# Kernel tuning notes

Measured on AMD Instinct MI355X. Metric: run time of the kernel, lower is better.

## Reference

```python
import jax, jax.numpy as jnp
import numpy as np
import math

B, T, D, H = 4, 1024, 1024, 16
DK = D // H
TAU_THRESH = 0.3


def setup_inputs() -> dict:
    key = jax.random.key(0)
    ks = jax.random.split(key, 13)
    s = 1.0 / math.sqrt(D)
    return {
        "x": jax.random.normal(ks[0], (B, T, D), dtype=jnp.float32),
        "Wq": jax.random.normal(ks[1], (D, D), dtype=jnp.float32) * s,
        "bq": jax.random.normal(ks[2], (D,), dtype=jnp.float32) * s,
        "Wk": jax.random.normal(ks[3], (D, D), dtype=jnp.float32) * s,
        "bk": jax.random.normal(ks[4], (D,), dtype=jnp.float32) * s,
        "Wv": jax.random.normal(ks[5], (D, D), dtype=jnp.float32) * s,
        "bv": jax.random.normal(ks[6], (D,), dtype=jnp.float32) * s,
        "Wo": jax.random.normal(ks[7], (D, D), dtype=jnp.float32) * s,
        "bo": jax.random.normal(ks[8], (D,), dtype=jnp.float32) * s,
        "Wg1": jax.random.normal(ks[9], (1, D), dtype=jnp.float32) * s,
        "bg1": jax.random.normal(ks[10], (1,), dtype=jnp.float32) * s,
        "Wg2": jax.random.normal(ks[11], (1, D), dtype=jnp.float32) * s,
        "bg2": jax.random.normal(ks[12], (1,), dtype=jnp.float32) * s,
    }


def reference(x, Wq, bq, Wk, bk, Wv, bv, Wo, bo, Wg1, bg1, Wg2, bg2):
    b, t, d = x.shape
    # projections (torch Linear: y = x @ W.T + b)
    Q = (x @ Wq.T + bq).reshape(b, t, H, DK).transpose(0, 2, 1, 3)  # [B,H,T,dk]
    K = (x @ Wk.T + bk).reshape(b, t, H, DK).transpose(0, 2, 1, 3)
    V = (x @ Wv.T + bv).reshape(b, t, H, DK).transpose(0, 2, 1, 3)
    scores = jnp.einsum("bhqd,bhkd->bhqk", Q, K) / math.sqrt(DK)  # [B,H,T,T]
    # confidence gates from first-token query context [B, H*dk] = [B, D]
    context = Q[:, :, 0, :].reshape(b, d)
    q1 = jax.nn.sigmoid(context @ Wg1.T + bg1)  # [B,1]
    q2 = jax.nn.sigmoid(context @ Wg2.T + bg2)  # [B,1]
    c = jnp.clip(q1 * q2, 1e-8, 1.0)            # [B,1]
    tau = jnp.where(c < TAU_THRESH, 1.0 / c, jnp.ones_like(c)).reshape(b, 1, 1, 1)
    p = jax.nn.softmax(scores / tau, axis=-1)
    cb = c.reshape(b, 1, 1, 1)
    p_gated = cb * p + (1.0 - cb) * (1.0 / t)
    u = jnp.mean(1.0 - c, axis=-1, keepdims=True)  # [B,1]
    attn_out = jnp.einsum("bhqk,bhkd->bhqd", p_gated, V)
    attn_out = attn_out.transpose(0, 2, 1, 3).reshape(b, t, d)
    output = attn_out @ Wo.T + bo
    return output, u
```

## Files before the change

### kernel.cpp

```cpp
#include <hip/hip_runtime.h>
#include <stdint.h>

typedef short bf16x8 __attribute__((ext_vector_type(8)));
typedef float f32x4 __attribute__((ext_vector_type(4)));

#define MFMA_BF16(a, b, c) __builtin_amdgcn_mfma_f32_16x16x32_bf16((a), (b), (c), 0, 0, 0)

__device__ __forceinline__ short f2bf(float x) {
  union { float f; uint32_t u; } v; v.f = x;
  uint32_t r = (v.u + 0x7FFFu + ((v.u >> 16) & 1u)) >> 16;
  return (short)r;
}
__device__ __forceinline__ uint32_t rnd_bf_hi(float x) {
  union { float f; uint32_t u; } v; v.f = x;
  return v.u + 0x7FFFu + ((v.u >> 16) & 1u);
}
__device__ __forceinline__ uint32_t pack2bf(float a, float b) {
  return __builtin_amdgcn_perm(rnd_bf_hi(b), rnd_bf_hi(a), 0x07060302);
}
__device__ __forceinline__ float bfbits2f(uint32_t b16) {
  union { uint32_t u; float f; } v; v.u = b16 << 16; return v.f;
}
__device__ __forceinline__ float fexp2(float x) {
#if __has_builtin(__builtin_amdgcn_exp2f)
  return __builtin_amdgcn_exp2f(x);
#else
  return __expf(x * 0.6931471805599453f);
#endif
}
__device__ __forceinline__ void async16(const void* g, void* l) {
  __builtin_amdgcn_global_load_lds(
      (const __attribute__((address_space(1))) uint32_t*)g,
      (__attribute__((address_space(3))) uint32_t*)l, 16, 0, 0);
}

__global__ __launch_bounds__(256) void prep_k(
    const float* __restrict__ x, const float* __restrict__ Wq,
    const float* __restrict__ Wk, const float* __restrict__ Wv,
    const float* __restrict__ Wo, const float* __restrict__ bq,
    short* __restrict__ xb, short* __restrict__ Wqb, short* __restrict__ Wkb,
    short* __restrict__ Wvb, short* __restrict__ Wob, float* __restrict__ ctx) {
  __shared__ float xs[1024];
  const int bid = blockIdx.x;
  const int tid = threadIdx.x;
  if (bid < 8192) {
    const float* src; short* dst; int idx;
    if (bid < 4096) {
      src = x; dst = xb; idx = (bid << 8) + tid;
    } else {
      const int r = bid - 4096;
      const int z = r >> 10;
      src = (z == 0) ? Wq : (z == 1) ? Wk : (z == 2) ? Wv : Wo;
      dst = (z == 0) ? Wqb : (z == 1) ? Wkb : (z == 2) ? Wvb : Wob;
      idx = ((r & 1023) << 8) + tid;
    }
    float4 v = ((const float4*)src)[idx];
    short4 o;
    o.x = f2bf(v.x); o.y = f2bf(v.y); o.z = f2bf(v.z); o.w = f2bf(v.w);
    ((short4*)dst)[idx] = o;
  } else {
    const int r = bid - 8192;
    const int b = r >> 4;
    const int n0 = (r & 15) << 6;
    for (int i = tid; i < 1024; i += 256) xs[i] = x[b * 1048576 + i];
    __syncthreads();
    const int w = tid >> 6, lane = tid & 63;
    const float4* xv4 = (const float4*)xs;
    for (int rr = 0; rr < 16; ++rr) {
      const int n = n0 + (w << 4) + rr;
      const float4* wrow = (const float4*)(Wq + n * 1024);
      float p = 0.f;
#pragma unroll
      for (int c2 = 0; c2 < 4; ++c2) {
        float4 wv = wrow[lane + (c2 << 6)];
        float4 xv = xv4[lane + (c2 << 6)];
        p += xv.x * wv.x + xv.y * wv.y + xv.z * wv.z + xv.w * wv.w;
      }
#pragma unroll
      for (int off = 32; off; off >>= 1) p += __shfl_xor(p, off);
      if (lane == 0) ctx[b * 1024 + n] = p + bq[n];
    }
  }
}

__global__ __launch_bounds__(256) void gates_fin(const float* __restrict__ ctx,
                                                 const float* __restrict__ Wg1,
                                                 const float* __restrict__ bg1,
                                                 const float* __restrict__ Wg2,
                                                 const float* __restrict__ bg2,
                                                 float* __restrict__ gates,
                                                 float* __restrict__ u_out) {
  __shared__ float red[16];
  const int tid = threadIdx.x, w = tid >> 6, lane = tid & 63;
  for (int b = 0; b < 4; ++b) {
    float4 cv = ((const float4*)(ctx + b * 1024))[tid];
    float4 w1 = ((const float4*)Wg1)[tid];
    float4 w2 = ((const float4*)Wg2)[tid];
    float p1 = cv.x * w1.x + cv.y * w1.y + cv.z * w1.z + cv.w * w1.w;
    float p2 = cv.x * w2.x + cv.y * w2.y + cv.z * w2.z + cv.w * w2.w;
#pragma unroll
    for (int off = 32; off; off >>= 1) { p1 += __shfl_xor(p1, off); p2 += __shfl_xor(p2, off); }
    if (lane == 0) { red[w] = p1; red[8 + w] = p2; }
    __syncthreads();
    if (tid == 0) {
      float g1 = red[0] + red[1] + red[2] + red[3] + bg1[0];
      float g2 = red[8] + red[9] + red[10] + red[11] + bg2[0];
      float q1 = 1.f / (1.f + expf(-g1));
      float q2 = 1.f / (1.f + expf(-g2));
      float c = fminf(fmaxf(q1 * q2, 1e-8f), 1.0f);
      gates[b * 2 + 0] = c;
      gates[b * 2 + 1] = (c < 0.3f ? c : 1.0f) * 0.125f * 1.4426950408889634f;
      u_out[b] = 1.0f - c;
    }
    __syncthreads();
  }
}

__global__ __launch_bounds__(256) void gemm_qkv(
    const short* __restrict__ xb,
    const short* __restrict__ Wqb, const short* __restrict__ Wkb, const short* __restrict__ Wvb,
    const float* __restrict__ bq, const float* __restrict__ bk, const float* __restrict__ bv,
    short* __restrict__ Qh, short* __restrict__ Kh, short* __restrict__ Vt) {
  const int z = blockIdx.z;
  const short* W = (z == 0) ? Wqb : (z == 1) ? Wkb : Wvb;
  const float* bias = (z == 0) ? bq : (z == 1) ? bk : bv;

  const int m0 = blockIdx.x << 7;
  const int n0 = blockIdx.y << 7;
  const int tid = threadIdx.x;
  const int w = tid >> 6, lane = tid & 63;
  const int m15 = lane & 15, quad = lane >> 4;
  const int wr = w >> 1, wc = w & 1;

  __shared__ short As[4096];
  __shared__ short Bs[4096];

  f32x4 acc[4][4];
#pragma unroll
  for (int i = 0; i < 4; ++i)
#pragma unroll
    for (int j = 0; j < 4; ++j) { f32x4 zz = {0.f, 0.f, 0.f, 0.f}; acc[i][j] = zz; }

  const int srow = (w << 5) + (lane >> 2);
  const int scol = (lane & 3) << 3;
  const short* ga0 = xb + (m0 + srow) * 1024 + scol;
  const short* ga1 = ga0 + 16 * 1024;
  const short* gb0 = W + (n0 + srow) * 1024 + scol;
  const short* gb1 = gb0 + 16 * 1024;
  short* la0 = &As[srow * 32 + scol];
  short* la1 = la0 + 512;
  short* lb0 = &Bs[srow * 32 + scol];
  short* lb1 = lb0 + 512;

  for (int kt = 0; kt < 32; ++kt) {
    async16(ga0, la0); async16(ga1, la1);
    async16(gb0, lb0); async16(gb1, lb1);
    ga0 += 32; ga1 += 32; gb0 += 32; gb1 += 32;
    __syncthreads();
    bf16x8 a[4], b[4];
#pragma unroll
    for (int i = 0; i < 4; ++i)
      a[i] = *(const bf16x8*)(&As[((wr << 6) + (i << 4) + m15) * 32 + (quad << 3)]);
#pragma unroll
    for (int j = 0; j < 4; ++j)
      b[j] = *(const bf16x8*)(&Bs[((wc << 6) + (j << 4) + m15) * 32 + (quad << 3)]);
#pragma unroll
    for (int i = 0; i < 4; ++i)
#pragma unroll
      for (int j = 0; j < 4; ++j)
        acc[i][j] = MFMA_BF16(a[i], b[j], acc[i][j]);
    __syncthreads();
  }

#pragma unroll
  for (int j = 0; j < 4; ++j) {
    const int n = n0 + (wc << 6) + (j << 4) + m15;
    const float bb_ = bias[n];
    const int h = n >> 6, dk = n & 63;
#pragma unroll
    for (int i = 0; i < 4; ++i) {
      const int mb = m0 + (wr << 6) + (i << 4) + (quad << 2);
#pragma unroll
      for (int r = 0; r < 4; ++r) {
        const int m = mb + r;
        const int batch = m >> 10, t = m & 1023;
        const short o = f2bf(acc[i][j][r] + bb_);
        if (z == 2) {
          Vt[((batch * 16 + h) * 64 + dk) * 1024 + t] = o;
        } else if (z == 1) {
          Kh[((batch * 16 + h) * 1024 + t) * 64 + dk] = o;
        } else {
          Qh[((batch * 16 + h) * 1024 + t) * 64 + dk] = o;
        }
      }
    }
  }
}

__global__ __launch_bounds__(256) void gemm_out(const short* __restrict__ Ab,
                                                const short* __restrict__ Wo,
                                                const float* __restrict__ bo,
                                                float* __restrict__ Cout) {
  const int m0 = blockIdx.x << 6;
  const int n0 = blockIdx.y << 7;
  const int tid = threadIdx.x;
  const int w = tid >> 6, lane = tid & 63;
  const int m15 = lane & 15, quad = lane >> 4;
  const int wr = w >> 1, wc = w & 1;

  __shared__ short As[2048];
  __shared__ short Bs[4096];

  f32x4 acc[2][4];
#pragma unroll
  for (int i = 0; i < 2; ++i)
#pragma unroll
    for (int j = 0; j < 4; ++j) { f32x4 zz = {0.f, 0.f, 0.f, 0.f}; acc[i][j] = zz; }

  const int s0 = tid, s1 = tid + 256;
  const int arow = s0 >> 2, alcb = (s0 & 3) ^ ((arow >> 1) & 3);
  const int brow1 = s1 >> 2, blcb1 = (s1 & 3) ^ ((brow1 >> 1) & 3);
  const short* gA  = Ab + (m0 + arow) * 1024 + (alcb << 3);
  const short* gB0 = Wo + (n0 + arow) * 1024 + (alcb << 3);
  const short* gB1 = Wo + (n0 + brow1) * 1024 + (blcb1 << 3);
  short* lA  = &As[s0 << 3];
  short* lB0 = &Bs[s0 << 3];
  short* lB1 = &Bs[s1 << 3];

  for (int kt = 0; kt < 32; ++kt) {
    async16(gA, lA);
    async16(gB0, lB0); async16(gB1, lB1);
    gA += 32; gB0 += 32; gB1 += 32;
    __syncthreads();
    bf16x8 a[2], b[4];
#pragma unroll
    for (int i = 0; i < 2; ++i) {
      const int ra = (wr << 5) + (i << 4) + m15;
      a[i] = *(const bf16x8*)(&As[ra * 32 + ((quad ^ ((ra >> 1) & 3)) << 3)]);
    }
#pragma unroll
    for (int j = 0; j < 4; ++j) {
      const int rb = (wc << 6) + (j << 4) + m15;
      b[j] = *(const bf16x8*)(&Bs[rb * 32 + ((quad ^ ((rb >> 1) & 3)) << 3)]);
    }
#pragma unroll
    for (int i = 0; i < 2; ++i)
#pragma unroll
      for (int j = 0; j < 4; ++j)
        acc[i][j] = MFMA_BF16(a[i], b[j], acc[i][j]);
    __syncthreads();
  }

#pragma unroll
  for (int j = 0; j < 4; ++j) {
    const int n = n0 + (wc << 6) + (j << 4) + m15;
    const float bb_ = bo[n];
#pragma unroll
    for (int i = 0; i < 2; ++i) {
      const int mb = m0 + (wr << 5) + (i << 4) + (quad << 2);
#pragma unroll
      for (int r = 0; r < 4; ++r)
        Cout[(mb + r) * 1024 + n] = acc[i][j][r] + bb_;
    }
  }
}

__global__ __launch_bounds__(256) void meanv_k(const short* __restrict__ Vt,
                                               float* __restrict__ mV) {
  const int bh = blockIdx.x;
  const int tid = threadIdx.x;
  const int d = tid >> 2, part = tid & 3;
  const short* row = Vt + bh * 65536 + d * 1024 + part * 256;
  float s = 0.f;
#pragma unroll 4
  for (int i = 0; i < 64; ++i) {
    uint2 v = *(const uint2*)(row + i * 4);
    s += bfbits2f(v.x & 0xffffu) + bfbits2f(v.x >> 16) +
         bfbits2f(v.y & 0xffffu) + bfbits2f(v.y >> 16);
  }
  s += __shfl_xor(s, 1);
  s += __shfl_xor(s, 2);
  if (part == 0) mV[bh * 64 + d] = s;
}

__global__ __launch_bounds__(256, 4) void attn_k(const short* __restrict__ Qh,
                                                 const short* __restrict__ Kh,
                                                 const short* __restrict__ Vt,
                                                 const float* __restrict__ gates,
                                                 const float* __restrict__ mV,
                                                 short* __restrict__ attnb) {
  const int bh = blockIdx.x;
  const int b = bh >> 4, h = bh & 15;
  const int q0 = blockIdx.y << 6;
  const int tid = threadIdx.x;
  const int w = tid >> 6, lane = tid & 63;
  const int m15 = lane & 15, quad = lane >> 4;

  __shared__ short Ks[2][4096];
  __shared__ short Vs[2][4096];

  const short* ksrc = Kh + bh * 65536;
  const short* vsrc = Vt + bh * 65536;

  const float sl = gates[b * 2 + 1];

  const short* qsrc = Qh + ((bh << 10) + q0 + (w << 4) + m15) * 64;
  const bf16x8 qb0 = *(const bf16x8*)(qsrc + (quad << 3));
  const bf16x8 qb1 = *(const bf16x8*)(qsrc + 32 + (quad << 3));

  const int off0 = tid, off1 = tid + 256;
  const int r0 = off0 >> 3, cb0 = (off0 & 7) ^ (r0 & 7);
  const int r1 = off1 >> 3, cb1 = (off1 & 7) ^ (r1 & 7);

#define STAGE(kv, bufi)                                                        \
  do {                                                                         \
    async16(ksrc + (((kv) << 6) + r0) * 64 + (cb0 << 3), &Ks[bufi][off0 << 3]);\
    async16(ksrc + (((kv) << 6) + r1) * 64 + (cb1 << 3), &Ks[bufi][off1 << 3]);\
    async16(vsrc + r0 * 1024 + ((kv) << 6) + (cb0 << 3), &Vs[bufi][off0 << 3]);\
    async16(vsrc + r1 * 1024 + ((kv) << 6) + (cb1 << 3), &Vs[bufi][off1 << 3]);\
  } while (0)

  STAGE(0, 0);

  float lsum = 0.f;
  f32x4 o_acc[4];
#pragma unroll
  for (int jd = 0; jd < 4; ++jd) { f32x4 zz = {0.f, 0.f, 0.f, 0.f}; o_acc[jd] = zz; }

  const int srcA = ((quad & 1) << 5) + m15;
  const int srcB = srcA + 16;
  const bool selhi = (quad & 2) != 0;

  for (int kv = 0; kv < 16; ++kv) {
    __syncthreads();
    if (kv < 15) STAGE(kv + 1, (kv + 1) & 1);
    const short* Kb = &Ks[kv & 1][0];
    const short* Vb = &Vs[kv & 1][0];

    f32x4 sacc[4];
#pragma unroll
    for (int s = 0; s < 4; ++s) {
      const int row = (s << 4) + m15;
      const int sw = row & 7;
      bf16x8 a0 = *(const bf16x8*)(Kb + (row << 6) + ((quad ^ sw) << 3));
      bf16x8 a1 = *(const bf16x8*)(Kb + (row << 6) + (((quad + 4) ^ sw) << 3));
      f32x4 zz = {0.f, 0.f, 0.f, 0.f};
      zz = MFMA_BF16(a0, qb0, zz);
      zz = MFMA_BF16(a1, qb1, zz);
      sacc[s] = zz;
    }

    uint32_t pk[4][2];
#pragma unroll
    for (int s = 0; s < 4; ++s) {
      float p0 = fexp2(sacc[s][0] * sl);
      float p1 = fexp2(sacc[s][1] * sl);
      float p2 = fexp2(sacc[s][2] * sl);
      float p3 = fexp2(sacc[s][3] * sl);
      lsum += (p0 + p1) + (p2 + p3);
      pk[s][0] = pack2bf(p0, p1);
      pk[s][1] = pack2bf(p2, p3);
    }

    bf16x8 pf[2];
#pragma unroll
    for (int H = 0; H < 2; ++H) {
      uint32_t f[4];
#pragma unroll
      for (int rp = 0; rp < 2; ++rp) {
        uint32_t alo = (uint32_t)__shfl((int)pk[2 * H][rp], srcA);
        uint32_t ahi = (uint32_t)__shfl((int)pk[2 * H + 1][rp], srcA);
        uint32_t blo = (uint32_t)__shfl((int)pk[2 * H][rp], srcB);
        uint32_t bhi = (uint32_t)__shfl((int)pk[2 * H + 1][rp], srcB);
        f[rp]     = selhi ? ahi : alo;
        f[2 + rp] = selhi ? bhi : blo;
      }
      pf[H] = *(bf16x8*)f;
    }

#pragma unroll
    for (int jd = 0; jd < 4; ++jd) {
      const int row = (jd << 4) + m15;
      const int sw = row & 7;
      bf16x8 v0 = *(const bf16x8*)(Vb + (row << 6) + ((quad ^ sw) << 3));
      bf16x8 v1 = *(const bf16x8*)(Vb + (row << 6) + (((quad + 4) ^ sw) << 3));
      o_acc[jd] = MFMA_BF16(v0, pf[0], o_acc[jd]);
      o_acc[jd] = MFMA_BF16(v1, pf[1], o_acc[jd]);
    }
  }
#undef STAGE

  float l = lsum;
  l += __shfl_xor(l, 16);
  l += __shfl_xor(l, 32);

  const float cg = gates[b * 2 + 0];
  const float s0 = cg / l;
  const float coef = (1.0f - cg) * (1.0f / 1024.0f);
  const int qrow = q0 + (w << 4) + m15;
  short* orow = attnb + ((b << 10) + qrow) * 1024 + (h << 6);
#pragma unroll
  for (int jd = 0; jd < 4; ++jd) {
    float4 mv = *(const float4*)(mV + (bh << 6) + (jd << 4) + (quad << 2));
    float v0_ = s0 * o_acc[jd][0] + coef * mv.x;
    float v1_ = s0 * o_acc[jd][1] + coef * mv.y;
    float v2_ = s0 * o_acc[jd][2] + coef * mv.z;
    float v3_ = s0 * o_acc[jd][3] + coef * mv.w;
    uint2 st;
    st.x = pack2bf(v0_, v1_);
    st.y = pack2bf(v2_, v3_);
    *(uint2*)(orow + (jd << 4) + (quad << 2)) = st;
  }
}

extern "C" void kernel_launch(void* const* d_in, const int* in_sizes, int n_in,
                              void* d_out, int out_size, void* d_ws, size_t ws_size,
                              hipStream_t stream) {
  const float* x   = (const float*)d_in[0];
  const float* Wq  = (const float*)d_in[1];
  const float* bq  = (const float*)d_in[2];
  const float* Wk  = (const float*)d_in[3];
  const float* bk  = (const float*)d_in[4];
  const float* Wv  = (const float*)d_in[5];
  const float* bv  = (const float*)d_in[6];
  const float* Wo  = (const float*)d_in[7];
  const float* bo  = (const float*)d_in[8];
  const float* Wg1 = (const float*)d_in[9];
  const float* bg1 = (const float*)d_in[10];
  const float* Wg2 = (const float*)d_in[11];
  const float* bg2 = (const float*)d_in[12];
  float* out = (float*)d_out;

  char* ws = (char*)d_ws;
  short* xb   = (short*)(ws + 0);
  short* Wqb  = (short*)(ws + 8388608);
  short* Wkb  = (short*)(ws + 10485760);
  short* Wvb  = (short*)(ws + 12582912);
  short* Wob  = (short*)(ws + 14680064);
  short* Qh   = (short*)(ws + 16777216);
  short* Kh   = (short*)(ws + 25165824);
  short* Vt   = (short*)(ws + 33554432);
  short* attb = (short*)(ws + 41943040);
  float* ctx  = (float*)(ws + 50331648);
  float* gat  = (float*)(ws + 50348032);
  float* mV   = (float*)(ws + 50348064);

  prep_k<<<8256, 256, 0, stream>>>(x, Wq, Wk, Wv, Wo, bq,
                                   xb, Wqb, Wkb, Wvb, Wob, ctx);
  gates_fin<<<1, 256, 0, stream>>>(ctx, Wg1, bg1, Wg2, bg2, gat, out + 4194304);

  gemm_qkv<<<dim3(32, 8, 3), 256, 0, stream>>>(xb, Wqb, Wkb, Wvb, bq, bk, bv,
                                               Qh, Kh, Vt);
  meanv_k<<<64, 256, 0, stream>>>(Vt, mV);
  attn_k<<<dim3(64, 16), 256, 0, stream>>>(Qh, Kh, Vt, gat, mV, attb);
  gemm_out<<<dim3(64, 8), 256, 0, stream>>>(attb, Wob, bo, out);
}
```

Measured before the change: 212.5 us.

## Split attention over key blocks with separate combine kernel

Attention is split across two key halves (grid z=2), so each block runs 8 KV tiles instead of 16. The launch bound rises to 8 blocks per SM and the LDS double buffer becomes a single buffer with synchronous staging. Partial fp32 outputs and row sums are written to workspace, and a new combine kernel sums them and applies the gate mix. This doubles the number of blocks to fill more CUs, at the cost of losing the copy/compute overlap and adding an extra launch plus an ~32MB fp32 partial round trip.

New measurement: 223.9 us. +5.4%, slower.

```diff
diff --git a/kernel.cpp b/kernel.cpp
--- a/kernel.cpp
+++ b/kernel.cpp
@@ -283,21 +283,23 @@
   if (part == 0) mV[bh * 64 + d] = s;
 }
 
-__global__ __launch_bounds__(256, 4) void attn_k(const short* __restrict__ Qh,
-                                                 const short* __restrict__ Kh,
-                                                 const short* __restrict__ Vt,
-                                                 const float* __restrict__ gates,
-                                                 const float* __restrict__ mV,
-                                                 short* __restrict__ attnb) {
+__global__ __launch_bounds__(256, 8) void attn_part(const short* __restrict__ Qh,
+                                                    const short* __restrict__ Kh,
+                                                    const short* __restrict__ Vt,
+                                                    const float* __restrict__ gates,
+                                                    float* __restrict__ Op,
+                                                    float* __restrict__ Lp) {
   const int bh = blockIdx.x;
-  const int b = bh >> 4, h = bh & 15;
+  const int b = bh >> 4;
   const int q0 = blockIdx.y << 6;
+  const int z = blockIdx.z;
+  const int kvb = z << 3;
   const int tid = threadIdx.x;
   const int w = tid >> 6, lane = tid & 63;
   const int m15 = lane & 15, quad = lane >> 4;
 
-  __shared__ short Ks[2][4096];
-  __shared__ short Vs[2][4096];
+  __shared__ short Ks[4096];
+  __shared__ short Vs[4096];
 
   const short* ksrc = Kh + bh * 65536;
   const short* vsrc = Vt + bh * 65536;
@@ -312,16 +314,6 @@
   const int r0 = off0 >> 3, cb0 = (off0 & 7) ^ (r0 & 7);
   const int r1 = off1 >> 3, cb1 = (off1 & 7) ^ (r1 & 7);
 
-#define STAGE(kv, bufi)                                                        \
-  do {                                                                         \
-    async16(ksrc + (((kv) << 6) + r0) * 64 + (cb0 << 3), &Ks[bufi][off0 << 3]);\
-    async16(ksrc + (((kv) << 6) + r1) * 64 + (cb1 << 3), &Ks[bufi][off1 << 3]);\
-    async16(vsrc + r0 * 1024 + ((kv) << 6) + (cb0 << 3), &Vs[bufi][off0 << 3]);\
-    async16(vsrc + r1 * 1024 + ((kv) << 6) + (cb1 << 3), &Vs[bufi][off1 << 3]);\
-  } while (0)
-
-  STAGE(0, 0);
-
   float lsum = 0.f;
   f32x4 o_acc[4];
 #pragma unroll
@@ -331,19 +323,21 @@
   const int srcB = srcA + 16;
   const bool selhi = (quad & 2) != 0;
 
-  for (int kv = 0; kv < 16; ++kv) {
-    __syncthreads();
-    if (kv < 15) STAGE(kv + 1, (kv + 1) & 1);
-    const short* Kb = &Ks[kv & 1][0];
-    const short* Vb = &Vs[kv & 1][0];
+  for (int kv = 0; kv < 8; ++kv) {
+    const int kt = kvb + kv;
+    async16(ksrc + ((kt << 6) + r0) * 64 + (cb0 << 3), &Ks[off0 << 3]);
+    async16(ksrc + ((kt << 6) + r1) * 64 + (cb1 << 3), &Ks[off1 << 3]);
+    async16(vsrc + r0 * 1024 + (kt << 6) + (cb0 << 3), &Vs[off0 << 3]);
+    async16(vsrc + r1 * 1024 + (kt << 6) + (cb1 << 3), &Vs[off1 << 3]);
+    __syncthreads();
 
     f32x4 sacc[4];
 #pragma unroll
     for (int s = 0; s < 4; ++s) {
       const int row = (s << 4) + m15;
       const int sw = row & 7;
-      bf16x8 a0 = *(const bf16x8*)(Kb + (row << 6) + ((quad ^ sw) << 3));
-      bf16x8 a1 = *(const bf16x8*)(Kb + (row << 6) + (((quad + 4) ^ sw) << 3));
+      bf16x8 a0 = *(const bf16x8*)(Ks + (row << 6) + ((quad ^ sw) << 3));
+      bf16x8 a1 = *(const bf16x8*)(Ks + (row << 6) + (((quad + 4) ^ sw) << 3));
       f32x4 zz = {0.f, 0.f, 0.f, 0.f};
       zz = MFMA_BF16(a0, qb0, zz);
       zz = MFMA_BF16(a1, qb1, zz);
@@ -382,35 +376,61 @@
     for (int jd = 0; jd < 4; ++jd) {
       const int row = (jd << 4) + m15;
       const int sw = row & 7;
-      bf16x8 v0 = *(const bf16x8*)(Vb + (row << 6) + ((quad ^ sw) << 3));
-      bf16x8 v1 = *(const bf16x8*)(Vb + (row << 6) + (((quad + 4) ^ sw) << 3));
+      bf16x8 v0 = *(const bf16x8*)(Vs + (row << 6) + ((quad ^ sw) << 3));
+      bf16x8 v1 = *(const bf16x8*)(Vs + (row << 6) + (((quad + 4) ^ sw) << 3));
       o_acc[jd] = MFMA_BF16(v0, pf[0], o_acc[jd]);
       o_acc[jd] = MFMA_BF16(v1, pf[1], o_acc[jd]);
     }
-  }
-#undef STAGE
+    __syncthreads();
+  }
 
   float l = lsum;
   l += __shfl_xor(l, 16);
   l += __shfl_xor(l, 32);
 
+  const int qrow = q0 + (w << 4) + m15;
+  float* op = Op + ((((z << 6) + bh) << 10) + qrow) * 64;
+#pragma unroll
+  for (int jd = 0; jd < 4; ++jd)
+    *(f32x4*)(op + (jd << 4) + (quad << 2)) = o_acc[jd];
+  if (quad == 0) Lp[(((z << 6) + bh) << 10) + qrow] = l;
+}
+
+__global__ __launch_bounds__(256) void attn_comb(const float* __restrict__ Op,
+                                                 const float* __restrict__ Lp,
+                                                 const float* __restrict__ gates,
+                                                 const float* __restrict__ mV,
+                                                 short* __restrict__ attnb) {
+  const int bh = blockIdx.x, qt = blockIdx.y;
+  const int b = bh >> 4, h = bh & 15;
+  const int tid = threadIdx.x;
+  const int q = tid >> 2, db = (tid & 3) << 4;
+  const int qrow = (qt << 6) + q;
+
   const float cg = gates[b * 2 + 0];
+  const float coef = (1.0f - cg) * (1.0f / 1024.0f);
+  const float l = Lp[(bh << 10) + qrow] + Lp[((64 + bh) << 10) + qrow];
   const float s0 = cg / l;
-  const float coef = (1.0f - cg) * (1.0f / 1024.0f);
-  const int qrow = q0 + (w << 4) + m15;
-  short* orow = attnb + ((b << 10) + qrow) * 1024 + (h << 6);
-#pragma unroll
-  for (int jd = 0; jd < 4; ++jd) {
-    float4 mv = *(const float4*)(mV + (bh << 6) + (jd << 4) + (quad << 2));
-    float v0_ = s0 * o_acc[jd][0] + coef * mv.x;
-    float v1_ = s0 * o_acc[jd][1] + coef * mv.y;
-    float v2_ = s0 * o_acc[jd][2] + coef * mv.z;
-    float v3_ = s0 * o_acc[jd][3] + coef * mv.w;
-    uint2 st;
-    st.x = pack2bf(v0_, v1_);
-    st.y = pack2bf(v2_, v3_);
-    *(uint2*)(orow + (jd << 4) + (quad << 2)) = st;
-  }
+
+  const float* o0 = Op + (((bh) << 10) + qrow) * 64 + db;
+  const float* o1 = o0 + (64 << 10) * 64;
+  short* orow = attnb + (((b << 10) + qrow) << 10) + (h << 6) + db;
+
+  uint32_t outw[8];
+#pragma unroll
+  for (int c4 = 0; c4 < 4; ++c4) {
+    float4 a  = ((const float4*)o0)[c4];
+    float4 bb = ((const float4*)o1)[c4];
+    float4 mv = *(const float4*)(mV + (bh << 6) + db + (c4 << 2));
+    float r0 = s0 * (a.x + bb.x) + coef * mv.x;
+    float r1 = s0 * (a.y + bb.y) + coef * mv.y;
+    float r2 = s0 * (a.z + bb.z) + coef * mv.z;
+    float r3 = s0 * (a.w + bb.w) + coef * mv.w;
+    outw[c4 * 2]     = pack2bf(r0, r1);
+    outw[c4 * 2 + 1] = pack2bf(r2, r3);
+  }
+  *(uint4*)orow       = *(uint4*)&outw[0];
+  *(uint4*)(orow + 8) = *(uint4*)&outw[4];
 }
 
 extern "C" void kernel_launch(void* const* d_in, const int* in_sizes, int n_in,
@@ -444,6 +464,8 @@
   float* ctx  = (float*)(ws + 50331648);
   float* gat  = (float*)(ws + 50348032);
   float* mV   = (float*)(ws + 50348064);
+  float* Op   = (float*)(ws + 50397184);
+  float* Lp   = (float*)(ws + 83951616);
 
   prep_k<<<8256, 256, 0, stream>>>(x, Wq, Wk, Wv, Wo, bq,
                                    xb, Wqb, Wkb, Wvb, Wob, ctx);
@@ -452,6 +474,7 @@
   gemm_qkv<<<dim3(32, 8, 3), 256, 0, stream>>>(xb, Wqb, Wkb, Wvb, bq, bk, bv,
                                                Qh, Kh, Vt);
   meanv_k<<<64, 256, 0, stream>>>(Vt, mV);
-  attn_k<<<dim3(64, 16), 256, 0, stream>>>(Qh, Kh, Vt, gat, mV, attb);
+  attn_part<<<dim3(64, 16, 2), 256, 0, stream>>>(Qh, Kh, Vt, gat, Op, Lp);
+  attn_comb<<<dim3(64, 16), 256, 0, stream>>>(Op, Lp, gat, mV, attb);
   gemm_out<<<dim3(64, 8), 256, 0, stream>>>(attb, Wob, bo, out);
 }
```

## Split attention KV range across two warp groups and widen QKV GEMM k-tile

Applied to the files above, without the earlier changes.

The attention kernel now launches 512 threads per block: two 256-thread groups each process half of the key/value tiles for the same 64 queries. Their partial outputs and row sums are combined through shared memory before the gated epilogue. The double-buffered prefetch is replaced by load-then-sync per tile, which adds more barriers and gives up overlap in exchange for twice the waves per query block. Separately, the QKV GEMM uses a 64-wide k-tile with an XOR-swizzled LDS layout, halving loop iterations and barriers and avoiding bank conflicts.

After: 229.7 us. 1.08x slower.

```diff
diff --git a/kernel.cpp b/kernel.cpp
--- a/kernel.cpp
+++ b/kernel.cpp
@@ -132,8 +132,8 @@
   const int m15 = lane & 15, quad = lane >> 4;
   const int wr = w >> 1, wc = w & 1;
 
-  __shared__ short As[4096];
-  __shared__ short Bs[4096];
+  __shared__ short As[8192];
+  __shared__ short Bs[8192];
 
   f32x4 acc[4][4];
 #pragma unroll
@@ -141,34 +141,46 @@
 #pragma unroll
     for (int j = 0; j < 4; ++j) { f32x4 zz = {0.f, 0.f, 0.f, 0.f}; acc[i][j] = zz; }
 
-  const int srow = (w << 5) + (lane >> 2);
-  const int scol = (lane & 3) << 3;
-  const short* ga0 = xb + (m0 + srow) * 1024 + scol;
-  const short* ga1 = ga0 + 16 * 1024;
-  const short* gb0 = W + (n0 + srow) * 1024 + scol;
-  const short* gb1 = gb0 + 16 * 1024;
-  short* la0 = &As[srow * 32 + scol];
-  short* la1 = la0 + 512;
-  short* lb0 = &Bs[srow * 32 + scol];
-  short* lb1 = lb0 + 512;
-
-  for (int kt = 0; kt < 32; ++kt) {
-    async16(ga0, la0); async16(ga1, la1);
-    async16(gb0, lb0); async16(gb1, lb1);
-    ga0 += 32; ga1 += 32; gb0 += 32; gb1 += 32;
-    __syncthreads();
-    bf16x8 a[4], b[4];
-#pragma unroll
-    for (int i = 0; i < 4; ++i)
-      a[i] = *(const bf16x8*)(&As[((wr << 6) + (i << 4) + m15) * 32 + (quad << 3)]);
-#pragma unroll
-    for (int j = 0; j < 4; ++j)
-      b[j] = *(const bf16x8*)(&Bs[((wc << 6) + (j << 4) + m15) * 32 + (quad << 3)]);
-#pragma unroll
-    for (int i = 0; i < 4; ++i)
-#pragma unroll
-      for (int j = 0; j < 4; ++j)
-        acc[i][j] = MFMA_BF16(a[i], b[j], acc[i][j]);
+  const short* gA[4];
+  const short* gB[4];
+  short* lA[4];
+  short* lB[4];
+#pragma unroll
+  for (int i = 0; i < 4; ++i) {
+    const int s = tid + (i << 8);
+    const int row = s >> 3;
+    const int cb = (s & 7) ^ (row & 7);
+    gA[i] = xb + (m0 + row) * 1024 + (cb << 3);
+    gB[i] = W + (n0 + row) * 1024 + (cb << 3);
+    lA[i] = &As[s << 3];
+    lB[i] = &Bs[s << 3];
+  }
+
+  for (int kt = 0; kt < 16; ++kt) {
+#pragma unroll
+    for (int i = 0; i < 4; ++i) { async16(gA[i], lA[i]); async16(gB[i], lB[i]); }
+#pragma unroll
+    for (int i = 0; i < 4; ++i) { gA[i] += 64; gB[i] += 64; }
+    __syncthreads();
+#pragma unroll
+    for (int h = 0; h < 2; ++h) {
+      bf16x8 a[4], b[4];
+#pragma unroll
+      for (int i = 0; i < 4; ++i) {
+        const int ra = (wr << 6) + (i << 4) + m15;
+        a[i] = *(const bf16x8*)(&As[(ra << 6) + ((((h << 2) + quad) ^ (ra & 7)) << 3)]);
+      }
+#pragma unroll
+      for (int j = 0; j < 4; ++j) {
+        const int rb = (wc << 6) + (j << 4) + m15;
+        b[j] = *(const bf16x8*)(&Bs[(rb << 6) + ((((h << 2) + quad) ^ (rb & 7)) << 3)]);
+      }
+#pragma unroll
+      for (int i = 0; i < 4; ++i)
+#pragma unroll
+        for (int j = 0; j < 4; ++j)
+          acc[i][j] = MFMA_BF16(a[i], b[j], acc[i][j]);
+    }
     __syncthreads();
   }
 
@@ -283,7 +295,7 @@
   if (part == 0) mV[bh * 64 + d] = s;
 }
 
-__global__ __launch_bounds__(256, 4) void attn_k(const short* __restrict__ Qh,
+__global__ __launch_bounds__(512, 6) void attn_k(const short* __restrict__ Qh,
                                                  const short* __restrict__ Kh,
                                                  const short* __restrict__ Vt,
                                                  const float* __restrict__ gates,
@@ -293,34 +305,28 @@
   const int b = bh >> 4, h = bh & 15;
   const int q0 = blockIdx.y << 6;
   const int tid = threadIdx.x;
-  const int w = tid >> 6, lane = tid & 63;
+  const int g = tid >> 8;
+  const int t8 = tid & 255;
+  const int w = t8 >> 6, lane = t8 & 63;
   const int m15 = lane & 15, quad = lane >> 4;
 
-  __shared__ short Ks[2][4096];
-  __shared__ short Vs[2][4096];
+  __shared__ short KV[2][8192];
+  __shared__ float l1s[64];
+
+  short* Ks = &KV[g][0];
+  short* Vs = &KV[g][4096];
 
   const short* ksrc = Kh + bh * 65536;
   const short* vsrc = Vt + bh * 65536;
-
   const float sl = gates[b * 2 + 1];
 
   const short* qsrc = Qh + ((bh << 10) + q0 + (w << 4) + m15) * 64;
   const bf16x8 qb0 = *(const bf16x8*)(qsrc + (quad << 3));
   const bf16x8 qb1 = *(const bf16x8*)(qsrc + 32 + (quad << 3));
 
-  const int off0 = tid, off1 = tid + 256;
+  const int off0 = t8, off1 = t8 + 256;
   const int r0 = off0 >> 3, cb0 = (off0 & 7) ^ (r0 & 7);
   const int r1 = off1 >> 3, cb1 = (off1 & 7) ^ (r1 & 7);
-
-#define STAGE(kv, bufi)                                                        \
-  do {                                                                         \
-    async16(ksrc + (((kv) << 6) + r0) * 64 + (cb0 << 3), &Ks[bufi][off0 << 3]);\
-    async16(ksrc + (((kv) << 6) + r1) * 64 + (cb1 << 3), &Ks[bufi][off1 << 3]);\
-    async16(vsrc + r0 * 1024 + ((kv) << 6) + (cb0 << 3), &Vs[bufi][off0 << 3]);\
-    async16(vsrc + r1 * 1024 + ((kv) << 6) + (cb1 << 3), &Vs[bufi][off1 << 3]);\
-  } while (0)
-
-  STAGE(0, 0);
 
   float lsum = 0.f;
   f32x4 o_acc[4];
@@ -331,19 +337,21 @@
   const int srcB = srcA + 16;
   const bool selhi = (quad & 2) != 0;
 
-  for (int kv = 0; kv < 16; ++kv) {
-    __syncthreads();
-    if (kv < 15) STAGE(kv + 1, (kv + 1) & 1);
-    const short* Kb = &Ks[kv & 1][0];
-    const short* Vb = &Vs[kv & 1][0];
+  for (int kv = 0; kv < 8; ++kv) {
+    const int kt = (g << 3) + kv;
+    async16(ksrc + ((kt << 6) + r0) * 64 + (cb0 << 3), Ks + (off0 << 3));
+    async16(ksrc + ((kt << 6) + r1) * 64 + (cb1 << 3), Ks + (off1 << 3));
+    async16(vsrc + r0 * 1024 + (kt << 6) + (cb0 << 3), Vs + (off0 << 3));
+    async16(vsrc + r1 * 1024 + (kt << 6) + (cb1 << 3), Vs + (off1 << 3));
+    __syncthreads();
 
     f32x4 sacc[4];
 #pragma unroll
     for (int s = 0; s < 4; ++s) {
       const int row = (s << 4) + m15;
       const int sw = row & 7;
-      bf16x8 a0 = *(const bf16x8*)(Kb + (row << 6) + ((quad ^ sw) << 3));
-      bf16x8 a1 = *(const bf16x8*)(Kb + (row << 6) + (((quad + 4) ^ sw) << 3));
+      bf16x8 a0 = *(const bf16x8*)(Ks + (row << 6) + ((quad ^ sw) << 3));
+      bf16x8 a1 = *(const bf16x8*)(Ks + (row << 6) + (((quad + 4) ^ sw) << 3));
       f32x4 zz = {0.f, 0.f, 0.f, 0.f};
       zz = MFMA_BF16(a0, qb0, zz);
       zz = MFMA_BF16(a1, qb1, zz);
@@ -382,34 +390,46 @@
     for (int jd = 0; jd < 4; ++jd) {
       const int row = (jd << 4) + m15;
       const int sw = row & 7;
-      bf16x8 v0 = *(const bf16x8*)(Vb + (row << 6) + ((quad ^ sw) << 3));
-      bf16x8 v1 = *(const bf16x8*)(Vb + (row << 6) + (((quad + 4) ^ sw) << 3));
+      bf16x8 v0 = *(const bf16x8*)(Vs + (row << 6) + ((quad ^ sw) << 3));
+      bf16x8 v1 = *(const bf16x8*)(Vs + (row << 6) + (((quad + 4) ^ sw) << 3));
       o_acc[jd] = MFMA_BF16(v0, pf[0], o_acc[jd]);
       o_acc[jd] = MFMA_BF16(v1, pf[1], o_acc[jd]);
     }
-  }
-#undef STAGE
+    __syncthreads();
+  }
 
   float l = lsum;
   l += __shfl_xor(l, 16);
   l += __shfl_xor(l, 32);
 
-  const float cg = gates[b * 2 + 0];
-  const float s0 = cg / l;
-  const float coef = (1.0f - cg) * (1.0f / 1024.0f);
-  const int qrow = q0 + (w << 4) + m15;
-  short* orow = attnb + ((b << 10) + qrow) * 1024 + (h << 6);
-#pragma unroll
-  for (int jd = 0; jd < 4; ++jd) {
-    float4 mv = *(const float4*)(mV + (bh << 6) + (jd << 4) + (quad << 2));
-    float v0_ = s0 * o_acc[jd][0] + coef * mv.x;
-    float v1_ = s0 * o_acc[jd][1] + coef * mv.y;
-    float v2_ = s0 * o_acc[jd][2] + coef * mv.z;
-    float v3_ = s0 * o_acc[jd][3] + coef * mv.w;
-    uint2 st;
-    st.x = pack2bf(v0_, v1_);
-    st.y = pack2bf(v2_, v3_);
-    *(uint2*)(orow + (jd << 4) + (quad << 2)) = st;
+  float* Ops = (float*)&KV[0][0];
+  const int q = (w << 4) + m15;
+  if (g == 1) {
+#pragma unroll
+    for (int jd = 0; jd < 4; ++jd)
+      *(f32x4*)&Ops[q * 68 + (jd << 4) + (quad << 2)] = o_acc[jd];
+    if (quad == 0) l1s[q] = l;
+  }
+  __syncthreads();
+  if (g == 0) {
+    const float lt = l + l1s[q];
+    const float cg = gates[b * 2 + 0];
+    const float s0 = cg / lt;
+    const float coef = (1.0f - cg) * (1.0f / 1024.0f);
+    short* orow = attnb + ((b << 10) + q0 + q) * 1024 + (h << 6);
+#pragma unroll
+    for (int jd = 0; jd < 4; ++jd) {
+      f32x4 o1 = *(const f32x4*)&Ops[q * 68 + (jd << 4) + (quad << 2)];
+      float4 mv = *(const float4*)(mV + (bh << 6) + (jd << 4) + (quad << 2));
+      float v0_ = s0 * (o_acc[jd][0] + o1[0]) + coef * mv.x;
+      float v1_ = s0 * (o_acc[jd][1] + o1[1]) + coef * mv.y;
+      float v2_ = s0 * (o_acc[jd][2] + o1[2]) + coef * mv.z;
+      float v3_ = s0 * (o_acc[jd][3] + o1[3]) + coef * mv.w;
+      uint2 st;
+      st.x = pack2bf(v0_, v1_);
+      st.y = pack2bf(v2_, v3_);
+      *(uint2*)(orow + (jd << 4) + (quad << 2)) = st;
+    }
   }
 }
 
@@ -452,6 +472,6 @@
   gemm_qkv<<<dim3(32, 8, 3), 256, 0, stream>>>(xb, Wqb, Wkb, Wvb, bq, bk, bv,
                                                Qh, Kh, Vt);
   meanv_k<<<64, 256, 0, stream>>>(Vt, mV);
-  attn_k<<<dim3(64, 16), 256, 0, stream>>>(Qh, Kh, Vt, gat, mV, attb);
+  attn_k<<<dim3(64, 16), 512, 0, stream>>>(Qh, Kh, Vt, gat, mV, attb);
   gemm_out<<<dim3(64, 8), 256, 0, stream>>>(attb, Wob, bo, out);
 }
```
